# Optimization experiments

Measured on AMD Instinct MI355X. Metric: run time of the kernel, lower is better.

## Reference

```python
import jax, jax.numpy as jnp
import numpy as np

LN_EPS = 1e-5

def _ln(x):
    # haiku LayerNorm([-1], create_scale=False, create_offset=False)
    mu = x.mean(axis=-1, keepdims=True)
    var = x.var(axis=-1, keepdims=True)
    return (x - mu) * jax.lax.rsqrt(var + LN_EPS)

def setup_inputs() -> dict:
    key = jax.random.key(0)
    ks = jax.random.split(key, 10)
    N, L, P = 512, 256, 64
    inp = {
        "local": jax.random.normal(ks[0], (N, L), jnp.float32),
        "pair": jax.random.normal(ks[1], (N, N, P), jnp.float32),
        "mask": jax.random.randint(ks[2], (N,), 0, 2, jnp.int32),
        "W_pair_gate": jax.random.normal(ks[3], (P, 2 * P), jnp.float32) / np.sqrt(P),
        "W_pair_value": jax.random.normal(ks[4], (P, 2 * P), jnp.float32) / np.sqrt(P),
        "W_left_gate": jax.random.normal(ks[5], (L, 2 * P), jnp.float32) / np.sqrt(L),
        "W_left_value": jax.random.normal(ks[6], (L, 2 * P), jnp.float32) / np.sqrt(L),
        "W_right_gate": jax.random.normal(ks[7], (L, 2 * P), jnp.float32) / np.sqrt(L),
        "W_right_value": jax.random.normal(ks[8], (L, 2 * P), jnp.float32) / np.sqrt(L),
        "W_out": jax.random.normal(ks[9], (3 * P, P), jnp.float32) / np.sqrt(3 * P),
    }
    return inp

def reference(local, pair, mask, W_pair_gate, W_pair_value, W_left_gate,
              W_left_value, W_right_gate, W_right_value, W_out):
    maskb = mask.astype(bool)
    pair_mask = maskb[:, None] & maskb[None, :]                  # (N, N)
    l = _ln(local)                                               # (N, L)
    p = _ln(pair)                                                # (N, N, P)
    pair_gate = p @ W_pair_gate                                  # (N, N, 2P)
    pair_value = p @ W_pair_value                                # (N, N, 2P)
    # left: broadcast local over axis 0/1, gelu-gate, mask, reduce over j
    left_gate = jax.nn.gelu((l @ W_left_gate)[:, None] + pair_gate)
    left_value = (l @ W_left_value)[None, :] + pair_value
    left = jnp.where(pair_mask[..., None], left_gate * left_value, 0).sum(axis=1)  # (N, 2P)
    right_gate = jax.nn.gelu((l @ W_right_gate)[None, :] + pair_gate)
    right_value = (l @ W_right_value)[:, None] + pair_value
    right = jnp.where(pair_mask[..., None], right_gate * right_value, 0).sum(axis=0)  # (N, 2P)
    paired_pseudo_local = _ln(left[:, None] + right[None, :])    # (N, N, 2P)
    pair_hidden = jnp.concatenate((p, paired_pseudo_local), axis=-1)  # (N, N, 3P)
    return pair_hidden @ W_out                                   # (N, N, P)
```

## Files before the change

kernel.cpp:

```cpp
#include <hip/hip_runtime.h>
#include <math.h>

#define LN_EPS 1e-5f


typedef __bf16 bf16x8 __attribute__((ext_vector_type(8)));
typedef float f32x16 __attribute__((ext_vector_type(16)));

__device__ __forceinline__ float gelu_f(float x) {
    float x2 = x * x;
    float e = __builtin_amdgcn_exp2f(x * fmaf(0.10294423f, x2, 2.3022079f));
    float r = __builtin_amdgcn_rcpf(e + 1.0f);
    return fmaf(-x, r, x);
}

__global__ __launch_bounds__(256) void kA(
    const float* __restrict__ loc,
    const float* __restrict__ Wlg, const float* __restrict__ Wlv,
    const float* __restrict__ Wrg, const float* __restrict__ Wrv,
    float* __restrict__ proj, const int* __restrict__ mask,
    int* __restrict__ act, float* __restrict__ left, float* __restrict__ right) {
    const int t = threadIdx.x;
    if (blockIdx.x == 64) {
        if (blockIdx.y == 1) {
            float4 z = {0.f, 0.f, 0.f, 0.f};
            for (int idx = t; idx < 16384; idx += 256) ((float4*)left)[idx] = z;
        } else if (blockIdx.y == 2) {
            float4 z = {0.f, 0.f, 0.f, 0.f};
            for (int idx = t; idx < 16384; idx += 256) ((float4*)right)[idx] = z;
        } else if (blockIdx.y == 0) {
            __shared__ int cnt_sh[8];
            const int lane = t & 63, wv = t >> 6;
            int msave[2];
            unsigned long long bsave[2];
#pragma unroll
            for (int ch = 0; ch < 2; ++ch) {
                int m = (mask[ch * 256 + t] != 0);
                unsigned long long b = __ballot(m);
                if (lane == 0) cnt_sh[ch * 4 + wv] = __popcll(b);
                msave[ch] = m;
                bsave[ch] = b;
            }
            __syncthreads();
#pragma unroll
            for (int ch = 0; ch < 2; ++ch) {
                int base = 0;
                for (int u = 0; u < ch * 4 + wv; ++u) base += cnt_sh[u];
                int pos = base + __popcll(bsave[ch] & ((1ull << lane) - 1ull));
                if (msave[ch]) act[1 + pos] = ch * 256 + t;
            }
            if (t == 0) {
                int ctot = 0;
                for (int u = 0; u < 8; ++u) ctot += cnt_sh[u];
                act[0] = ctot;
            }
        }
        return;
    }
    __shared__ float ln_sh[8][260];
    __shared__ float red_sh[128][9];
    const int i0 = blockIdx.x * 8;
    const int mat = blockIdx.y;
    const float* __restrict__ W = (mat == 0) ? Wlg : (mat == 1) ? Wlv
                                 : (mat == 2) ? Wrg : Wrv;
    {
        int row = t >> 5, l32 = t & 31;
        const float4* src = (const float4*)(loc + (i0 + row) * 256);
        float4 v0 = src[l32 * 2];
        float4 v1 = src[l32 * 2 + 1];
        float s = (v0.x + v0.y) + (v0.z + v0.w) + (v1.x + v1.y) + (v1.z + v1.w);
        float ss = v0.x * v0.x + v0.y * v0.y + v0.z * v0.z + v0.w * v0.w +
                   v1.x * v1.x + v1.y * v1.y + v1.z * v1.z + v1.w * v1.w;
#pragma unroll
        for (int off = 1; off < 32; off <<= 1) {
            s += __shfl_xor(s, off);
            ss += __shfl_xor(ss, off);
        }
        float mu = s * (1.f / 256.f);
        float rs = rsqrtf(ss * (1.f / 256.f) - mu * mu + LN_EPS);
        float4 o0, o1;
        o0.x = (v0.x - mu) * rs; o0.y = (v0.y - mu) * rs;
        o0.z = (v0.z - mu) * rs; o0.w = (v0.w - mu) * rs;
        o1.x = (v1.x - mu) * rs; o1.y = (v1.y - mu) * rs;
        o1.z = (v1.z - mu) * rs; o1.w = (v1.w - mu) * rs;
        *(float4*)&ln_sh[row][l32 * 8] = o0;
        *(float4*)&ln_sh[row][l32 * 8 + 4] = o1;
    }
    __syncthreads();

    const int n = t & 127;
    const int kh = t >> 7;
    float acc[8] = {0.f, 0.f, 0.f, 0.f, 0.f, 0.f, 0.f, 0.f};
#pragma unroll 2
    for (int c = 0; c < 32; ++c) {
        const int kc = kh * 128 + c * 4;
        float w0 = W[(kc + 0) * 128 + n];
        float w1 = W[(kc + 1) * 128 + n];
        float w2 = W[(kc + 2) * 128 + n];
        float w3 = W[(kc + 3) * 128 + n];
#pragma unroll
        for (int r = 0; r < 8; ++r) {
            float4 l4 = *(const float4*)&ln_sh[r][kc];
            acc[r] += l4.x * w0 + l4.y * w1 + l4.z * w2 + l4.w * w3;
        }
    }
    if (kh == 1) {
#pragma unroll
        for (int r = 0; r < 8; ++r) red_sh[n][r] = acc[r];
    }
    __syncthreads();
    if (kh == 0) {
#pragma unroll
        for (int r = 0; r < 8; ++r)
            proj[mat * 65536 + (i0 + r) * 128 + n] = acc[r] + red_sh[n][r];
    }
}

#define KB_TI 4
__global__ __launch_bounds__(256) void kB(
    const float* __restrict__ pair, const int* __restrict__ act,
    const float* __restrict__ Wg, const float* __restrict__ Wv,
    const float* __restrict__ lg, const float* __restrict__ lv,
    const float* __restrict__ rg, const float* __restrict__ rv,
    float* __restrict__ left, float* __restrict__ right) {
    __shared__ __bf16 A_sh[2][32][72];
    __shared__ int ji_sh[32];
    __shared__ int ii_sh[KB_TI];

    const int cnt = act[0];
    const int j0 = blockIdx.x * 32;
    const int ibase = blockIdx.y * KB_TI;
    if (j0 >= cnt || ibase >= cnt) return;
    const int nact = min(KB_TI, cnt - ibase);

    const int t = threadIdx.x;
    const int lane = t & 63;
    const int w = t >> 6;
    const int c = lane & 31;
    const int half = lane >> 5;
    const int n = w * 32 + c;

    if (t < 32) ji_sh[t] = act[1 + min(j0 + t, cnt - 1)];
    if (t >= 64 && t < 64 + KB_TI) ii_sh[t - 64] = act[1 + min(ibase + (t - 64), cnt - 1)];
    __syncthreads();

    bf16x8 bg[4], bv[4];
#pragma unroll
    for (int kt = 0; kt < 4; ++kt) {
        bf16x8 vg, vv;
#pragma unroll
        for (int e = 0; e < 8; ++e) {
            int kr = kt * 16 + half * 8 + e;
            vg[e] = (__bf16)Wg[kr * 128 + n];
            vv[e] = (__bf16)Wv[kr * 128 + n];
        }
        bg[kt] = vg; bv[kt] = vv;
    }

    float lvr[16], rgr[16];
    unsigned jmask = 0;
#pragma unroll
    for (int r = 0; r < 16; ++r) {
        int m = 4 * half + (r & 3) + 8 * (r >> 2);
        int j = ji_sh[m];
        lvr[r] = lv[j * 128 + n];
        rgr[r] = rg[j * 128 + n];
        if (j0 + m < cnt) jmask |= (1u << r);
    }

    const int srow = t >> 3;
    const int kseg = (t & 7) * 8;
    float4 p0, p1;
    float plg, prv;
    {
        int iF = ii_sh[0];
        const float* src = pair + ((size_t)iF * 512 + ji_sh[srow]) * 64 + kseg;
        p0 = *(const float4*)src;
        p1 = *(const float4*)(src + 4);
        plg = lg[iF * 128 + n];
        prv = rv[iF * 128 + n];
    }

    auto lnwrite = [&](int buf) {
        float s = (p0.x + p0.y) + (p0.z + p0.w) + (p1.x + p1.y) + (p1.z + p1.w);
        float ss = p0.x * p0.x + p0.y * p0.y + p0.z * p0.z + p0.w * p0.w +
                   p1.x * p1.x + p1.y * p1.y + p1.z * p1.z + p1.w * p1.w;
        s += __shfl_xor(s, 1); ss += __shfl_xor(ss, 1);
        s += __shfl_xor(s, 2); ss += __shfl_xor(ss, 2);
        s += __shfl_xor(s, 4); ss += __shfl_xor(ss, 4);
        float mu = s * (1.f / 64.f);
        float rs = rsqrtf(ss * (1.f / 64.f) - mu * mu + LN_EPS);
        bf16x8 o;
        o[0] = (__bf16)((p0.x - mu) * rs); o[1] = (__bf16)((p0.y - mu) * rs);
        o[2] = (__bf16)((p0.z - mu) * rs); o[3] = (__bf16)((p0.w - mu) * rs);
        o[4] = (__bf16)((p1.x - mu) * rs); o[5] = (__bf16)((p1.y - mu) * rs);
        o[6] = (__bf16)((p1.z - mu) * rs); o[7] = (__bf16)((p1.w - mu) * rs);
        *(bf16x8*)&A_sh[buf][srow][kseg] = o;
    };
    lnwrite(0);
    __syncthreads();

    float racc[16];
#pragma unroll
    for (int r = 0; r < 16; ++r) racc[r] = 0.f;

    for (int ii = 0; ii < nact; ++ii) {
        const int i = ii_sh[ii];
        const float lgi = plg;
        const float rvi = prv;
        if (ii + 1 < nact) {
            int iF = ii_sh[ii + 1];
            const float* src = pair + ((size_t)iF * 512 + ji_sh[srow]) * 64 + kseg;
            p0 = *(const float4*)src;
            p1 = *(const float4*)(src + 4);
            plg = lg[iF * 128 + n];
            prv = rv[iF * 128 + n];
        }

        f32x16 ag = {}; f32x16 av = {};
#pragma unroll
        for (int kt = 0; kt < 4; ++kt) {
            bf16x8 af = *(const bf16x8*)&A_sh[ii & 1][c][kt * 16 + half * 8];
            ag = __builtin_amdgcn_mfma_f32_32x32x16_bf16(af, bg[kt], ag, 0, 0, 0);
            av = __builtin_amdgcn_mfma_f32_32x32x16_bf16(af, bv[kt], av, 0, 0, 0);
        }

        float lsum = 0.f;
#pragma unroll
        for (int r = 0; r < 16; ++r) {
            float pg = ag[r], pv = av[r];
            float lres = gelu_f(lgi + pg) * (lvr[r] + pv);
            float rres = gelu_f(rgr[r] + pg) * (rvi + pv);
            lsum += ((jmask >> r) & 1) ? lres : 0.f;
            racc[r] += rres;
        }
        float tot = lsum + __shfl_xor(lsum, 32);
        if (lane < 32) atomicAdd(&left[i * 128 + n], tot);

        if (ii + 1 < nact) lnwrite((ii + 1) & 1);
        __syncthreads();
    }

#pragma unroll
    for (int r = 0; r < 16; ++r) {
        if ((jmask >> r) & 1) {
            int m = 4 * half + (r & 3) + 8 * (r >> 2);
            atomicAdd(&right[ji_sh[m] * 128 + n], racc[r]);
        }
    }
}

__global__ __launch_bounds__(256) void kD(
    const float* __restrict__ left, const float* __restrict__ right,
    const float* __restrict__ W_out,
    float* __restrict__ Aw, float* __restrict__ Bw,
    float* __restrict__ rsrm, float* __restrict__ cs) {
    const int bx = blockIdx.x;
    const int t = threadIdx.x;
    if (bx < 256) {
        __shared__ float l_sh[32][68];
        __shared__ float r_sh[32][68];
        const int tx = t & 15, ty = t >> 4;
        const int i0 = (bx & 15) * 32, j0 = (bx >> 4) * 32;
        float acc00 = 0.f, acc01 = 0.f, acc10 = 0.f, acc11 = 0.f;
        float sL0 = 0.f, ssL0 = 0.f, sL1 = 0.f, ssL1 = 0.f;
        float sR0 = 0.f, ssR0 = 0.f, sR1 = 0.f, ssR1 = 0.f;
        for (int kc = 0; kc < 128; kc += 64) {
            __syncthreads();
#pragma unroll
            for (int u = 0; u < 2; ++u) {
                int fi = t + u * 256;
                int row = fi >> 4, kq = (fi & 15) * 4;
                float4 lv4 = *(const float4*)(left + (i0 + row) * 128 + kc + kq);
                float4 rv4 = *(const float4*)(right + (j0 + row) * 128 + kc + kq);
                *(float4*)&l_sh[row][kq] = lv4;
                *(float4*)&r_sh[row][kq] = rv4;
            }
            __syncthreads();
#pragma unroll
            for (int k4 = 0; k4 < 64; k4 += 4) {
                float4 l0 = *(const float4*)&l_sh[ty * 2 + 0][k4];
                float4 l1 = *(const float4*)&l_sh[ty * 2 + 1][k4];
                float4 r0 = *(const float4*)&r_sh[tx * 2 + 0][k4];
                float4 r1 = *(const float4*)&r_sh[tx * 2 + 1][k4];
                acc00 += l0.x * r0.x + l0.y * r0.y + l0.z * r0.z + l0.w * r0.w;
                acc01 += l0.x * r1.x + l0.y * r1.y + l0.z * r1.z + l0.w * r1.w;
                acc10 += l1.x * r0.x + l1.y * r0.y + l1.z * r0.z + l1.w * r0.w;
                acc11 += l1.x * r1.x + l1.y * r1.y + l1.z * r1.z + l1.w * r1.w;
                sL0 += (l0.x + l0.y) + (l0.z + l0.w);
                ssL0 += l0.x * l0.x + l0.y * l0.y + l0.z * l0.z + l0.w * l0.w;
                sL1 += (l1.x + l1.y) + (l1.z + l1.w);
                ssL1 += l1.x * l1.x + l1.y * l1.y + l1.z * l1.z + l1.w * l1.w;
                sR0 += (r0.x + r0.y) + (r0.z + r0.w);
                ssR0 += r0.x * r0.x + r0.y * r0.y + r0.z * r0.z + r0.w * r0.w;
                sR1 += (r1.x + r1.y) + (r1.z + r1.w);
                ssR1 += r1.x * r1.x + r1.y * r1.y + r1.z * r1.z + r1.w * r1.w;
            }
        }
        {
            float sLa[2] = {sL0, sL1}, ssLa[2] = {ssL0, ssL1};
            float sRb[2] = {sR0, sR1}, ssRb[2] = {ssR0, ssR1};
            float accv[2][2] = {{acc00, acc01}, {acc10, acc11}};
#pragma unroll
            for (int a = 0; a < 2; ++a) {
#pragma unroll
                for (int b = 0; b < 2; ++b) {
                    float mu = (sLa[a] + sRb[b]) * (1.f / 128.f);
                    float var = fmaf(-mu, mu,
                                     (ssLa[a] + 2.f * accv[a][b] + ssRb[b]) * (1.f / 128.f));
                    float rs = rsqrtf(var + LN_EPS);
                    size_t idx = (size_t)(i0 + ty * 2 + a) * 512 + (j0 + tx * 2 + b);
                    float2 v; v.x = rs; v.y = rs * mu;
                    ((float2*)rsrm)[idx] = v;
                }
            }
        }
    } else {
        const int id = bx - 256;
        const int which = id >> 8;
        const int sub = t >> 7;
        const int tt = t & 127;
        const int r = (id & 255) * 2 + sub;
        const float* src = which ? right : left;
        __shared__ float row_sh[2][128];
        row_sh[sub][tt] = src[r * 128 + tt];
        __syncthreads();
        if (tt < 64) {
            float a = 0.f;
            const float* W2 = W_out + 64 * 64;
#pragma unroll 8
            for (int m = 0; m < 128; ++m) a += row_sh[sub][m] * W2[m * 64 + tt];
            (which ? Bw : Aw)[r * 64 + tt] = a;
        }
        if (id == 0 && t < 64) {
            float c0 = 0.f, c1 = 0.f;
            for (int k = 0; k < 64; ++k) c0 += W_out[k * 64 + t];
            for (int m = 0; m < 128; ++m) c1 += W_out[(64 + m) * 64 + t];
            cs[t] = c0;
            cs[64 + t] = c1;
        }
    }
}

__global__ __launch_bounds__(256) void kC(
    const float* __restrict__ pair, const float* __restrict__ Wout,
    const float* __restrict__ Aw, const float* __restrict__ Bw,
    const float* __restrict__ rsrm,
    const float* __restrict__ cs, float* __restrict__ out) {
    __shared__ float2 rsrm_sh[4][64];
    const int t = threadIdx.x;
    const int lane = t & 63;
    const int w = t >> 6;
    const int c = lane & 31;
    const int half = lane >> 5;
    const int i0 = blockIdx.x * 4;
    const int j0 = blockIdx.y * 64;
    const int mt = w & 1;
    const int nt = w >> 1;
    const int n = nt * 32 + c;
    const int jrow = j0 + mt * 32 + c;

    const float* __restrict__ abase = pair + ((size_t)i0 * 512 + jrow) * 64 + half * 8;

    float4 va[8], vb[8];
#pragma unroll
    for (int kt = 0; kt < 4; ++kt) {
        va[2 * kt] = *(const float4*)(abase + kt * 16);
        va[2 * kt + 1] = *(const float4*)(abase + kt * 16 + 4);
    }

    rsrm_sh[t >> 6][t & 63] =
        ((const float2*)rsrm)[(size_t)(i0 + (t >> 6)) * 512 + j0 + (t & 63)];

    bf16x8 bo[4];
#pragma unroll
    for (int kt = 0; kt < 4; ++kt) {
        bf16x8 bb;
#pragma unroll
        for (int e = 0; e < 8; ++e)
            bb[e] = (__bf16)Wout[(kt * 16 + half * 8 + e) * 64 + n];
        bo[kt] = bb;
    }
    float Bv[16];
#pragma unroll
    for (int r = 0; r < 16; ++r) {
        int jp = j0 + mt * 32 + 4 * half + (r & 3) + 8 * (r >> 2);
        Bv[r] = Bw[jp * 64 + n];
    }
    float Awr[4];
#pragma unroll
    for (int u = 0; u < 4; ++u) Awr[u] = Aw[(i0 + u) * 64 + n];
    const float cs1n = cs[64 + n];

    auto stats = [&](float4 (&buf)[8], float& rs_o, float& nmr_o) {
        float s = 0.f, ss = 0.f;
#pragma unroll
        for (int u = 0; u < 8; ++u) {
            s += (buf[u].x + buf[u].y) + (buf[u].z + buf[u].w);
            ss += buf[u].x * buf[u].x + buf[u].y * buf[u].y +
                  buf[u].z * buf[u].z + buf[u].w * buf[u].w;
        }
        s += __shfl_xor(s, 32);
        ss += __shfl_xor(ss, 32);
        float mu = s * (1.f / 64.f);
        float rs = rsqrtf(ss * (1.f / 64.f) - mu * mu + LN_EPS);
        rs_o = rs;
        nmr_o = -mu * rs;
    };

    float rsA, nmrA, rsB, nmrB;
    stats(va, rsA, nmrA);
    __syncthreads();

    auto body = [&](float4 (&cur)[8], float4 (&nxt)[8], int ii,
                    float rs_c, float nmr_c, float& rs_n, float& nmr_n) {
        if (ii < 3) {
            const float* src = abase + (size_t)(ii + 1) * 512 * 64;
#pragma unroll
            for (int kt = 0; kt < 4; ++kt) {
                nxt[2 * kt] = *(const float4*)(src + kt * 16);
                nxt[2 * kt + 1] = *(const float4*)(src + kt * 16 + 4);
            }
        }
        const int i = i0 + ii;
        const float A_in = Awr[ii];

        f32x16 acc = {};
#pragma unroll
        for (int kt = 0; kt < 4; ++kt) {
            bf16x8 af;
#pragma unroll
            for (int u = 0; u < 2; ++u) {
                float4 vv = cur[2 * kt + u];
                af[u * 4 + 0] = (__bf16)fmaf(vv.x, rs_c, nmr_c);
                af[u * 4 + 1] = (__bf16)fmaf(vv.y, rs_c, nmr_c);
                af[u * 4 + 2] = (__bf16)fmaf(vv.z, rs_c, nmr_c);
                af[u * 4 + 3] = (__bf16)fmaf(vv.w, rs_c, nmr_c);
            }
            acc = __builtin_amdgcn_mfma_f32_32x32x16_bf16(af, bo[kt], acc, 0, 0, 0);
        }

        if (ii < 3) stats(nxt, rs_n, nmr_n);

#pragma unroll
        for (int r = 0; r < 16; ++r) {
            int jl = mt * 32 + 4 * half + (r & 3) + 8 * (r >> 2);
            float2 rr = rsrm_sh[ii][jl];
            out[((size_t)i * 512 + j0 + jl) * 64 + n] =
                fmaf(rr.x, A_in + Bv[r], fmaf(-rr.y, cs1n, acc[r]));
        }
    };
    body(va, vb, 0, rsA, nmrA, rsB, nmrB);
    body(vb, va, 1, rsB, nmrB, rsA, nmrA);
    body(va, vb, 2, rsA, nmrA, rsB, nmrB);
    body(vb, va, 3, rsB, nmrB, rsA, nmrA);
}

extern "C" void kernel_launch(void* const* d_in, const int* in_sizes, int n_in,
                              void* d_out, int out_size, void* d_ws, size_t ws_size,
                              hipStream_t stream) {
    const float* loc  = (const float*)d_in[0];
    const float* pair = (const float*)d_in[1];
    const int*   mask = (const int*)d_in[2];
    const float* Wpg  = (const float*)d_in[3];
    const float* Wpv  = (const float*)d_in[4];
    const float* Wlg  = (const float*)d_in[5];
    const float* Wlv  = (const float*)d_in[6];
    const float* Wrg  = (const float*)d_in[7];
    const float* Wrv  = (const float*)d_in[8];
    const float* Wout = (const float*)d_in[9];
    float* out = (float*)d_out;
    float* ws = (float*)d_ws;

    float* proj   = ws;
    float* left   = ws + 262144;
    float* right  = ws + 327680;
    float* Aw     = ws + 393216;
    float* Bw     = ws + 425984;
    float* rsrm   = ws + 458752;
    float* cs     = ws + 983040;
    int*   act    = (int*)(ws + 983168);

    kA<<<dim3(65, 4), 256, 0, stream>>>(loc, Wlg, Wlv, Wrg, Wrv, proj,
                                        mask, act, left, right);
    kB<<<dim3(16, 128), 256, 0, stream>>>(pair, act, Wpg, Wpv,
                                          proj, proj + 65536, proj + 131072,
                                          proj + 196608, left, right);
    kD<<<768, 256, 0, stream>>>(left, right, Wout, Aw, Bw, rsrm, cs);
    kC<<<dim3(128, 8), 256, 0, stream>>>(pair, Wout, Aw, Bw, rsrm, cs, out);
}
```

Before: 200.4 us.

## Stage pair tiles into LDS via async global_load_lds with swizzled double buffer

Kernel kC no longer loads pair rows straight into registers with double-buffered float4 prefetch. It now issues asynchronous global-to-LDS loads into a swizzled double-buffered shared tile and reads fragments back from LDS. LayerNorm stats are computed per iteration from the LDS data. The aim is to cut register pressure and improve load coalescing and latency hiding. The cost is 32KB of LDS per block, which may lower occupancy, plus an extra __syncthreads per iteration.

```diff
diff --git a/kernel.cpp b/kernel.cpp
--- a/kernel.cpp
+++ b/kernel.cpp
@@ -12,6 +12,13 @@
     float e = __builtin_amdgcn_exp2f(x * fmaf(0.10294423f, x2, 2.3022079f));
     float r = __builtin_amdgcn_rcpf(e + 1.0f);
     return fmaf(-x, r, x);
+}
+
+__device__ __forceinline__ void gload_lds16(const float* g, float* lds_base) {
+    __builtin_amdgcn_global_load_lds(
+        (const __attribute__((address_space(1))) unsigned int*)g,
+        (__attribute__((address_space(3))) unsigned int*)lds_base,
+        16, 0, 0);
 }
 
 __global__ __launch_bounds__(256) void kA(
@@ -347,6 +354,7 @@
     const float* __restrict__ Aw, const float* __restrict__ Bw,
     const float* __restrict__ rsrm,
     const float* __restrict__ cs, float* __restrict__ out) {
+    __shared__ float tile[2][64][64];
     __shared__ float2 rsrm_sh[4][64];
     const int t = threadIdx.x;
     const int lane = t & 63;
@@ -358,17 +366,20 @@
     const int mt = w & 1;
     const int nt = w >> 1;
     const int n = nt * 32 + c;
-    const int jrow = j0 + mt * 32 + c;
-
-    const float* __restrict__ abase = pair + ((size_t)i0 * 512 + jrow) * 64 + half * 8;
-
-    float4 va[8], vb[8];
-#pragma unroll
-    for (int kt = 0; kt < 4; ++kt) {
-        va[2 * kt] = *(const float4*)(abase + kt * 16);
-        va[2 * kt + 1] = *(const float4*)(abase + kt * 16 + 4);
-    }
-
+
+    auto stage = [&](int ii) {
+        float* dst0 = &tile[ii & 1][0][0];
+        const size_t gbase = ((size_t)(i0 + ii) * 512 + j0) * 64;
+#pragma unroll
+        for (int q = 0; q < 4; ++q) {
+            int row = w * 16 + q * 4 + (lane >> 4);
+            int gkb = ((lane & 15) << 4) ^ ((row & 7) << 4);
+            gload_lds16(pair + gbase + row * 64 + (gkb >> 2),
+                        dst0 + (w * 16 + q * 4) * 64);
+        }
+    };
+
+    stage(0);
     rsrm_sh[t >> 6][t & 63] =
         ((const float2*)rsrm)[(size_t)(i0 + (t >> 6)) * 512 + j0 + (t & 63)];
 
@@ -392,56 +403,55 @@
     for (int u = 0; u < 4; ++u) Awr[u] = Aw[(i0 + u) * 64 + n];
     const float cs1n = cs[64 + n];
 
-    auto stats = [&](float4 (&buf)[8], float& rs_o, float& nmr_o) {
+    const int jl_me = mt * 32 + c;
+    const int sw = (jl_me & 7) << 4;
+    const char* rowp = (const char*)&tile[0][jl_me][0];
+    const int tstride = (int)sizeof(float) * 64 * 64;
+
+    __syncthreads();
+
+    auto body = [&](int ii) {
+        if (ii < 3) stage(ii + 1);
+
+        const char* rp = rowp + (ii & 1) * tstride;
+        float4 f[8];
+#pragma unroll
+        for (int kt = 0; kt < 4; ++kt) {
+            int K = half * 32 + kt * 64;
+            f[2 * kt] = *(const float4*)(rp + (K ^ sw));
+            f[2 * kt + 1] = *(const float4*)(rp + ((K + 16) ^ sw));
+        }
+
         float s = 0.f, ss = 0.f;
 #pragma unroll
         for (int u = 0; u < 8; ++u) {
-            s += (buf[u].x + buf[u].y) + (buf[u].z + buf[u].w);
-            ss += buf[u].x * buf[u].x + buf[u].y * buf[u].y +
-                  buf[u].z * buf[u].z + buf[u].w * buf[u].w;
+            s += (f[u].x + f[u].y) + (f[u].z + f[u].w);
+            ss += f[u].x * f[u].x + f[u].y * f[u].y +
+                  f[u].z * f[u].z + f[u].w * f[u].w;
         }
         s += __shfl_xor(s, 32);
         ss += __shfl_xor(ss, 32);
         float mu = s * (1.f / 64.f);
         float rs = rsqrtf(ss * (1.f / 64.f) - mu * mu + LN_EPS);
-        rs_o = rs;
-        nmr_o = -mu * rs;
-    };
-
-    float rsA, nmrA, rsB, nmrB;
-    stats(va, rsA, nmrA);
-    __syncthreads();
-
-    auto body = [&](float4 (&cur)[8], float4 (&nxt)[8], int ii,
-                    float rs_c, float nmr_c, float& rs_n, float& nmr_n) {
-        if (ii < 3) {
-            const float* src = abase + (size_t)(ii + 1) * 512 * 64;
-#pragma unroll
-            for (int kt = 0; kt < 4; ++kt) {
-                nxt[2 * kt] = *(const float4*)(src + kt * 16);
-                nxt[2 * kt + 1] = *(const float4*)(src + kt * 16 + 4);
-            }
-        }
+        float nmr = -mu * rs;
+
+        f32x16 acc = {};
+#pragma unroll
+        for (int kt = 0; kt < 4; ++kt) {
+            bf16x8 af;
+#pragma unroll
+            for (int u = 0; u < 2; ++u) {
+                float4 vv = f[2 * kt + u];
+                af[u * 4 + 0] = (__bf16)fmaf(vv.x, rs, nmr);
+                af[u * 4 + 1] = (__bf16)fmaf(vv.y, rs, nmr);
+                af[u * 4 + 2] = (__bf16)fmaf(vv.z, rs, nmr);
+                af[u * 4 + 3] = (__bf16)fmaf(vv.w, rs, nmr);
+            }
+            acc = __builtin_amdgcn_mfma_f32_32x32x16_bf16(af, bo[kt], acc, 0, 0, 0);
+        }
+
         const int i = i0 + ii;
         const float A_in = Awr[ii];
-
-        f32x16 acc = {};
-#pragma unroll
-        for (int kt = 0; kt < 4; ++kt) {
-            bf16x8 af;
-#pragma unroll
-            for (int u = 0; u < 2; ++u) {
-                float4 vv = cur[2 * kt + u];
-                af[u * 4 + 0] = (__bf16)fmaf(vv.x, rs_c, nmr_c);
-                af[u * 4 + 1] = (__bf16)fmaf(vv.y, rs_c, nmr_c);
-                af[u * 4 + 2] = (__bf16)fmaf(vv.z, rs_c, nmr_c);
-                af[u * 4 + 3] = (__bf16)fmaf(vv.w, rs_c, nmr_c);
-            }
-            acc = __builtin_amdgcn_mfma_f32_32x32x16_bf16(af, bo[kt], acc, 0, 0, 0);
-        }
-
-        if (ii < 3) stats(nxt, rs_n, nmr_n);
-
 #pragma unroll
         for (int r = 0; r < 16; ++r) {
             int jl = mt * 32 + 4 * half + (r & 3) + 8 * (r >> 2);
@@ -449,11 +459,12 @@
             out[((size_t)i * 512 + j0 + jl) * 64 + n] =
                 fmaf(rr.x, A_in + Bv[r], fmaf(-rr.y, cs1n, acc[r]));
         }
+        __syncthreads();
     };
-    body(va, vb, 0, rsA, nmrA, rsB, nmrB);
-    body(vb, va, 1, rsB, nmrB, rsA, nmrA);
-    body(va, vb, 2, rsA, nmrA, rsB, nmrB);
-    body(vb, va, 3, rsB, nmrB, rsA, nmrA);
+    body(0);
+    body(1);
+    body(2);
+    body(3);
 }
 
 extern "C" void kernel_launch(void* const* d_in, const int* in_sizes, int n_in,
```

After: 194.4 us. -3.0%, faster.
